# Optimization experiments

Hardware: AMD Instinct MI355X
Metric: run time of the kernel (lower is better)

The kernel has to match this reference:

```python
import jax, jax.numpy as jnp
import numpy as np
from jax import lax


def setup_inputs() -> dict:
    key = jax.random.key(0)
    k1, k2 = jax.random.split(key)
    L, B, D = 1024, 16, 1024
    x = jax.random.normal(k1, (L, B, D), dtype=jnp.float32)
    # weight maps n_in -> n_out*k with k=3 (n_in == n_out); small scale for stability
    weight = jax.random.normal(k2, (D, 3 * D), dtype=jnp.float32) * 0.05
    bias = jnp.zeros((2 * D,), dtype=jnp.float32)
    c0 = jnp.zeros((B, D), dtype=jnp.float32)
    return {"x": x, "weight": weight, "bias": bias, "c0": c0}


def reference(x, weight, bias, c0):
    # SRUCell forward, k == 3 (n_in == n_out), unidirectional, tanh activation,
    # no dropout masks (mask_h == NULL -> mask = 1).
    L, B, D = x.shape
    u = (x.reshape(L * B, D) @ weight).reshape(L, B, D, 3)
    b1 = bias[:D]
    b2 = bias[D:]
    u0 = u[..., 0]                                   # [L, B, D]
    g1 = jax.nn.sigmoid(u[..., 1] + b1)              # forget gate
    g2 = jax.nn.sigmoid(u[..., 2] + b2)              # reset/highway gate

    def step(c, inp):
        u0_t, g1_t, g2_t, x_t = inp
        c_new = (c - u0_t) * g1_t + u0_t             # c = c'*g1 + u0*(1-g1)
        h_t = (jnp.tanh(c_new) - x_t) * g2_t + x_t   # h = act(c)*g2 + x*(1-g2)
        return c_new, h_t

    c_last, h = lax.scan(step, c0, (u0, g1, g2, x))
    return h, c_last
```

## Files before the change

### kernel.cpp

```cpp
#include <hip/hip_runtime.h>

#define L_DIM 1024
#define B_DIM 16
#define D_DIM 1024
#define K_DIM 1024
#define N_DIM 3072
#define M_DIM (L_DIM * B_DIM)
#define CHAINS 16384
#define CHUNK 64
#define NCHUNK 16

typedef float f32x4 __attribute__((ext_vector_type(4)));
typedef __bf16 bf16x8 __attribute__((ext_vector_type(8)));
typedef unsigned short u16;
typedef unsigned int u32;

__device__ __forceinline__ u16 f2bf(float f) {
  u32 u = __float_as_uint(f);
  u = u + 0x7FFFu + ((u >> 16) & 1u);
  return (u16)(u >> 16);
}
__device__ __forceinline__ float bf2f(u16 v) {
  return __uint_as_float(((u32)v) << 16);
}
__device__ __forceinline__ float fexp(float v) {
  return __builtin_amdgcn_exp2f(v * 1.4426950408889634f);
}
__device__ __forceinline__ float sigm(float z) {
  return __builtin_amdgcn_rcpf(1.0f + fexp(-z));
}
__device__ __forceinline__ float ftanh(float v) {
  return 1.0f - 2.0f * __builtin_amdgcn_rcpf(1.0f + fexp(2.0f * v));
}

__global__ __launch_bounds__(256) void cvt_x_kernel(const float4* __restrict__ in,
                                                    ushort4* __restrict__ out, int n4) {
  int i = blockIdx.x * 256 + threadIdx.x;
  if (i < n4) {
    float4 v = in[i];
    ushort4 o;
    o.x = f2bf(v.x); o.y = f2bf(v.y); o.z = f2bf(v.z); o.w = f2bf(v.w);
    out[i] = o;
  }
}

__global__ __launch_bounds__(256) void cvt_w_kernel(const float* __restrict__ W,
                                                    u16* __restrict__ Wt) {
  __shared__ float tile[64][65];
  int c0 = blockIdx.x * 64;
  int r0 = blockIdx.y * 64;
  int tx = threadIdx.x & 63;
  int ty = threadIdx.x >> 6;
#pragma unroll
  for (int i = 0; i < 16; ++i) {
    int row = i * 4 + ty;
    tile[row][tx] = W[(size_t)(r0 + row) * N_DIM + c0 + tx];
  }
  __syncthreads();
#pragma unroll
  for (int i = 0; i < 16; ++i) {
    int crow = i * 4 + ty;
    int c = c0 + crow;
    int nprime = (c % 3) * D_DIM + (c / 3);
    Wt[(size_t)nprime * K_DIM + r0 + tx] = f2bf(tile[tx][crow]);
  }
}

__global__ __launch_bounds__(256) void gemm_kernel(const u16* __restrict__ A,
                                                   const u16* __restrict__ Bt,
                                                   u16* __restrict__ U) {
  __shared__ u16 lA[128 * 32];
  __shared__ u16 lB[128 * 32];
  const int tid = threadIdx.x;
  const int wave = tid >> 6;
  const int lane = tid & 63;
  const int wm = wave >> 1, wn = wave & 1;
  const int quad = lane >> 4, l16 = lane & 15;
  const int m0 = blockIdx.y * 128;
  const int n0 = blockIdx.x * 128;

  f32x4 acc[4][4] = {};

  const u16* gA = A + (size_t)(m0 + (tid >> 2)) * K_DIM + (tid & 3) * 8;
  const u16* gB = Bt + (size_t)(n0 + (tid >> 2)) * K_DIM + (tid & 3) * 8;
  u16* sA0 = lA + wave * 512;
  u16* sA1 = lA + 2048 + wave * 512;
  u16* sB0 = lB + wave * 512;
  u16* sB1 = lB + 2048 + wave * 512;

  const u16* rA = lA + (wm * 64 + l16) * 32 + quad * 8;
  const u16* rB = lB + (wn * 64 + l16) * 32 + quad * 8;

  for (int k0 = 0; k0 < K_DIM; k0 += 32) {
    __syncthreads();
    __builtin_amdgcn_global_load_lds((const __attribute__((address_space(1))) void*)(gA + k0),
                                     (__attribute__((address_space(3))) void*)sA0, 16, 0, 0);
    __builtin_amdgcn_global_load_lds((const __attribute__((address_space(1))) void*)(gA + (size_t)64 * K_DIM + k0),
                                     (__attribute__((address_space(3))) void*)sA1, 16, 0, 0);
    __builtin_amdgcn_global_load_lds((const __attribute__((address_space(1))) void*)(gB + k0),
                                     (__attribute__((address_space(3))) void*)sB0, 16, 0, 0);
    __builtin_amdgcn_global_load_lds((const __attribute__((address_space(1))) void*)(gB + (size_t)64 * K_DIM + k0),
                                     (__attribute__((address_space(3))) void*)sB1, 16, 0, 0);
    __syncthreads();

    bf16x8 af[4], bfr[4];
#pragma unroll
    for (int mt = 0; mt < 4; ++mt) af[mt] = *(const bf16x8*)(rA + mt * 16 * 32);
#pragma unroll
    for (int nt = 0; nt < 4; ++nt) bfr[nt] = *(const bf16x8*)(rB + nt * 16 * 32);
#pragma unroll
    for (int mt = 0; mt < 4; ++mt)
#pragma unroll
      for (int nt = 0; nt < 4; ++nt)
        acc[mt][nt] = __builtin_amdgcn_mfma_f32_16x16x32_bf16(af[mt], bfr[nt], acc[mt][nt], 0, 0, 0);
  }

#pragma unroll
  for (int mt = 0; mt < 4; ++mt) {
#pragma unroll
    for (int nt = 0; nt < 4; ++nt) {
      int col = n0 + wn * 64 + nt * 16 + l16;
      int rbase = m0 + wm * 64 + mt * 16 + quad * 4;
#pragma unroll
      for (int r = 0; r < 4; ++r) {
        U[(size_t)(rbase + r) * N_DIM + col] = f2bf(acc[mt][nt][r]);
      }
    }
  }
}


__global__ __launch_bounds__(256) void sru_phase1(const u16* __restrict__ U,
                                                  const float* __restrict__ bias,
                                                  float* __restrict__ Aarr,
                                                  float* __restrict__ Barr) {
  int tid = blockIdx.x * 256 + threadIdx.x;
  int chain = tid & (CHAINS - 1);
  int j = tid >> 14;
  int d = chain & (D_DIM - 1);
  int b = chain >> 10;
  float bb1 = bias[d];
  const u16* p = U + (size_t)(j * CHUNK * B_DIM + b) * N_DIM + d;
  float A = 1.0f, Bv = 0.0f;
#pragma unroll 4
  for (int s = 0; s < CHUNK; ++s) {
    float u0 = bf2f(p[0]);
    float g1 = sigm(bf2f(p[D_DIM]) + bb1);
    Bv = (Bv - u0) * g1 + u0;
    A *= g1;
    p += (size_t)B_DIM * N_DIM;
  }
  Aarr[tid] = A;
  Barr[tid] = Bv;
}

__global__ __launch_bounds__(256) void sru_phase2(const float* __restrict__ Aarr,
                                                  const float* __restrict__ Barr,
                                                  const float* __restrict__ c0,
                                                  float* __restrict__ Cin,
                                                  float* __restrict__ clast) {
  int chain = blockIdx.x * 256 + threadIdx.x;
  float As[NCHUNK], Bs[NCHUNK];
#pragma unroll
  for (int j = 0; j < NCHUNK; ++j) {
    As[j] = Aarr[j * CHAINS + chain];
    Bs[j] = Barr[j * CHAINS + chain];
  }
  float c = c0[chain];
#pragma unroll
  for (int j = 0; j < NCHUNK; ++j) {
    Cin[j * CHAINS + chain] = c;
    c = As[j] * c + Bs[j];
  }
  clast[chain] = c;
}

__global__ __launch_bounds__(256) void sru_phase3(const u16* __restrict__ U,
                                                  const float* __restrict__ x,
                                                  const float* __restrict__ bias,
                                                  const float* __restrict__ Cin,
                                                  float* __restrict__ h) {
  int tid = blockIdx.x * 256 + threadIdx.x;
  int chain = tid & (CHAINS - 1);
  int j = tid >> 14;
  int d = chain & (D_DIM - 1);
  int b = chain >> 10;
  float bb1 = bias[d];
  float bb2 = bias[D_DIM + d];
  float c = Cin[tid];
  size_t m0 = (size_t)(j * CHUNK * B_DIM + b);
  const u16* p = U + m0 * N_DIM + d;
  const float* xp = x + m0 * D_DIM + d;
  float* hp = h + m0 * D_DIM + d;
#pragma unroll 4
  for (int s = 0; s < CHUNK; ++s) {
    float u0 = bf2f(p[0]);
    float g1 = sigm(bf2f(p[D_DIM]) + bb1);
    float g2 = sigm(bf2f(p[2 * D_DIM]) + bb2);
    c = (c - u0) * g1 + u0;
    float xv = *xp;
    *hp = (ftanh(c) - xv) * g2 + xv;
    p += (size_t)B_DIM * N_DIM;
    xp += B_DIM * D_DIM;
    hp += B_DIM * D_DIM;
  }
}

extern "C" void kernel_launch(void* const* d_in, const int* in_sizes, int n_in,
                              void* d_out, int out_size, void* d_ws, size_t ws_size,
                              hipStream_t stream) {
  const float* x = (const float*)d_in[0];
  const float* W = (const float*)d_in[1];
  const float* bias = (const float*)d_in[2];
  const float* c0 = (const float*)d_in[3];
  float* out = (float*)d_out;

  char* ws = (char*)d_ws;
  u16* xb = (u16*)ws;
  u16* wt = (u16*)(ws + 33554432);
  u16* U = (u16*)(ws + 33554432 + 6291456);
  float* Aarr = (float*)ws;
  float* Barr = (float*)(ws + 1048576);
  float* Cin  = (float*)(ws + 2097152);

  cvt_x_kernel<<<16384, 256, 0, stream>>>((const float4*)x, (ushort4*)xb, M_DIM * K_DIM / 4);
  cvt_w_kernel<<<dim3(48, 16), 256, 0, stream>>>(W, wt);
  gemm_kernel<<<dim3(N_DIM / 128, M_DIM / 128), 256, 0, stream>>>(xb, wt, U);
  sru_phase1<<<CHAINS * NCHUNK / 256, 256, 0, stream>>>(U, bias, Aarr, Barr);
  sru_phase2<<<CHAINS / 256, 256, 0, stream>>>(Aarr, Barr, c0, Cin, out + (size_t)M_DIM * D_DIM);
  sru_phase3<<<CHAINS * NCHUNK / 256, 256, 0, stream>>>(U, x, bias, Cin, out);
}
```

Measured before the change: 298.5 us.

## Rewrite GEMM as 256x256 double-buffered pipelined tile with swizzled LDS

Replaces the simple 128x128, single-buffer, two-barrier-per-K-step GEMM with a 256x256 tile run by 512 threads and a BK of 64. Loads go straight from global memory into a double-buffered LDS layout with an XOR swizzle, and the next tile is prefetched while MFMAs work on the current one. Block ids are remapped so neighbouring blocks share operands in cache, and s_setprio is raised around MFMA bursts. The goal is to hide global-load latency, cut LDS bank conflicts and raise operand reuse per block. The cost is 128KB of LDS and a large accumulator register footprint, and the hand-counted vmcnt waits are fragile.

After: 276.0 us. -7.5%, faster.

```diff
diff --git a/kernel.cpp b/kernel.cpp
--- a/kernel.cpp
+++ b/kernel.cpp
@@ -66,69 +66,140 @@
   }
 }
 
-__global__ __launch_bounds__(256) void gemm_kernel(const u16* __restrict__ A,
-                                                   const u16* __restrict__ Bt,
-                                                   u16* __restrict__ U) {
-  __shared__ u16 lA[128 * 32];
-  __shared__ u16 lB[128 * 32];
+
+#define AS1 __attribute__((address_space(1)))
+#define AS3 __attribute__((address_space(3)))
+#define STAGE(gp, lp) do { \
+  __builtin_amdgcn_global_load_lds((const AS1 void*)(gp), (AS3 void*)(lp), 16, 0, 0); \
+  __builtin_amdgcn_global_load_lds((const AS1 void*)((gp) + (size_t)64 * K_DIM), \
+                                   (AS3 void*)((lp) + 4096), 16, 0, 0); \
+} while (0)
+
+#define QUAD(AI, JB, BF) \
+  _Pragma("unroll") \
+  for (int i = 0; i < 4; ++i) { \
+    _Pragma("unroll") \
+    for (int j = 0; j < 2; ++j) { \
+      acc[AI + i][JB + j] = __builtin_amdgcn_mfma_f32_16x16x32_bf16(aF[i][0], BF[j][0], acc[AI + i][JB + j], 0, 0, 0); \
+      acc[AI + i][JB + j] = __builtin_amdgcn_mfma_f32_16x16x32_bf16(aF[i][1], BF[j][1], acc[AI + i][JB + j], 0, 0, 0); \
+    } \
+  }
+
+__global__ __launch_bounds__(512, 2) void gemm_kernel(const u16* __restrict__ A,
+                                                      const u16* __restrict__ Bt,
+                                                      u16* __restrict__ U) {
+  __shared__ __align__(16) u16 sm[65536];
   const int tid = threadIdx.x;
   const int wave = tid >> 6;
   const int lane = tid & 63;
-  const int wm = wave >> 1, wn = wave & 1;
-  const int quad = lane >> 4, l16 = lane & 15;
-  const int m0 = blockIdx.y * 128;
-  const int n0 = blockIdx.x * 128;
-
-  f32x4 acc[4][4] = {};
-
-  const u16* gA = A + (size_t)(m0 + (tid >> 2)) * K_DIM + (tid & 3) * 8;
-  const u16* gB = Bt + (size_t)(n0 + (tid >> 2)) * K_DIM + (tid & 3) * 8;
-  u16* sA0 = lA + wave * 512;
-  u16* sA1 = lA + 2048 + wave * 512;
-  u16* sB0 = lB + wave * 512;
-  u16* sB1 = lB + 2048 + wave * 512;
-
-  const u16* rA = lA + (wm * 64 + l16) * 32 + quad * 8;
-  const u16* rB = lB + (wn * 64 + l16) * 32 + quad * 8;
-
-  for (int k0 = 0; k0 < K_DIM; k0 += 32) {
-    __syncthreads();
-    __builtin_amdgcn_global_load_lds((const __attribute__((address_space(1))) void*)(gA + k0),
-                                     (__attribute__((address_space(3))) void*)sA0, 16, 0, 0);
-    __builtin_amdgcn_global_load_lds((const __attribute__((address_space(1))) void*)(gA + (size_t)64 * K_DIM + k0),
-                                     (__attribute__((address_space(3))) void*)sA1, 16, 0, 0);
-    __builtin_amdgcn_global_load_lds((const __attribute__((address_space(1))) void*)(gB + k0),
-                                     (__attribute__((address_space(3))) void*)sB0, 16, 0, 0);
-    __builtin_amdgcn_global_load_lds((const __attribute__((address_space(1))) void*)(gB + (size_t)64 * K_DIM + k0),
-                                     (__attribute__((address_space(3))) void*)sB1, 16, 0, 0);
-    __syncthreads();
-
-    bf16x8 af[4], bfr[4];
-#pragma unroll
-    for (int mt = 0; mt < 4; ++mt) af[mt] = *(const bf16x8*)(rA + mt * 16 * 32);
-#pragma unroll
-    for (int nt = 0; nt < 4; ++nt) bfr[nt] = *(const bf16x8*)(rB + nt * 16 * 32);
-#pragma unroll
-    for (int mt = 0; mt < 4; ++mt)
-#pragma unroll
-      for (int nt = 0; nt < 4; ++nt)
-        acc[mt][nt] = __builtin_amdgcn_mfma_f32_16x16x32_bf16(af[mt], bfr[nt], acc[mt][nt], 0, 0, 0);
-  }
-
-#pragma unroll
-  for (int mt = 0; mt < 4; ++mt) {
-#pragma unroll
-    for (int nt = 0; nt < 4; ++nt) {
-      int col = n0 + wn * 64 + nt * 16 + l16;
-      int rbase = m0 + wm * 64 + mt * 16 + quad * 4;
-#pragma unroll
-      for (int r = 0; r < 4; ++r) {
-        U[(size_t)(rbase + r) * N_DIM + col] = f2bf(acc[mt][nt][r]);
-      }
-    }
-  }
-}
-
+  const int wm = wave >> 2;
+  const int wn = wave & 3;
+  const int quad = lane >> 4;
+  const int l16 = lane & 15;
+
+  const int flat = blockIdx.y * 12 + blockIdx.x;
+  const int swz = (flat & 7) * 96 + (flat >> 3);
+  const int m0 = (swz / 12) * 256;
+  const int n0 = (swz % 12) * 256;
+
+  const int rr = tid >> 3;
+  const int slot = (tid & 7) ^ (rr & 7);
+  const u16* gA = A + (size_t)(m0 + rr) * K_DIM + slot * 8;
+  const u16* gB = Bt + (size_t)(n0 + rr) * K_DIM + slot * 8;
+
+  u16* ldsA = sm + wave * 512;
+  u16* ldsB = sm + 32768 + wave * 512;
+
+  const int swzu = (l16 & 7) << 3;
+  const int c0 = (quad * 8) ^ swzu;
+  const int c1 = (32 + quad * 8) ^ swzu;
+  const u16* pA = sm + (wm * 128 + l16) * 64;
+  const u16* pB = sm + 32768 + (wn * 64 + l16) * 64;
+
+  f32x4 acc[8][4] = {};
+
+  STAGE(gA, ldsA);
+  STAGE(gA + (size_t)128 * K_DIM, ldsA + 8192);
+  STAGE(gB, ldsB);
+  STAGE(gB + (size_t)128 * K_DIM, ldsB + 8192);
+  STAGE(gB + 64, ldsB + 16384);
+  STAGE(gB + (size_t)128 * K_DIM + 64, ldsB + 16384 + 8192);
+  asm volatile("s_waitcnt vmcnt(0)" ::: "memory");
+  __builtin_amdgcn_s_barrier();
+
+  for (int u = 0; u < 16; ++u) {
+    const int buf = u & 1;
+    const int nb = buf ^ 1;
+    const u16* pAb = pA + buf * 16384;
+    const u16* pBb = pB + buf * 16384;
+    bf16x8 aF[4][2], bLo[2][2], bHi[2][2];
+
+#pragma unroll
+    for (int i = 0; i < 4; ++i) {
+      aF[i][0] = *(const bf16x8*)(pAb + i * 1024 + c0);
+      aF[i][1] = *(const bf16x8*)(pAb + i * 1024 + c1);
+    }
+#pragma unroll
+    for (int j = 0; j < 2; ++j) {
+      bLo[j][0] = *(const bf16x8*)(pBb + j * 1024 + c0);
+      bLo[j][1] = *(const bf16x8*)(pBb + j * 1024 + c1);
+    }
+    if (u < 15) STAGE(gA + (u + 1) * 64, ldsA + nb * 16384);
+    __builtin_amdgcn_s_barrier();
+    __builtin_amdgcn_s_setprio(1);
+    QUAD(0, 0, bLo)
+    __builtin_amdgcn_s_setprio(0);
+    __builtin_amdgcn_s_barrier();
+
+#pragma unroll
+    for (int j = 0; j < 2; ++j) {
+      bHi[j][0] = *(const bf16x8*)(pBb + (2 + j) * 1024 + c0);
+      bHi[j][1] = *(const bf16x8*)(pBb + (2 + j) * 1024 + c1);
+    }
+    if (u < 15) STAGE(gA + (size_t)128 * K_DIM + (u + 1) * 64, ldsA + nb * 16384 + 8192);
+    __builtin_amdgcn_s_barrier();
+    __builtin_amdgcn_s_setprio(1);
+    QUAD(0, 2, bHi)
+    __builtin_amdgcn_s_setprio(0);
+    __builtin_amdgcn_s_barrier();
+
+#pragma unroll
+    for (int i = 0; i < 4; ++i) {
+      aF[i][0] = *(const bf16x8*)(pAb + (4 + i) * 1024 + c0);
+      aF[i][1] = *(const bf16x8*)(pAb + (4 + i) * 1024 + c1);
+    }
+    if (u < 14) STAGE(gB + (u + 2) * 64, ldsB + buf * 16384);
+    __builtin_amdgcn_s_barrier();
+    __builtin_amdgcn_s_setprio(1);
+    QUAD(4, 2, bHi)
+    __builtin_amdgcn_s_setprio(0);
+    __builtin_amdgcn_s_barrier();
+
+    if (u < 14) {
+      STAGE(gB + (size_t)128 * K_DIM + (u + 2) * 64, ldsB + buf * 16384 + 8192);
+      asm volatile("s_waitcnt vmcnt(4)" ::: "memory");
+    } else if (u == 14) {
+      asm volatile("s_waitcnt vmcnt(0)" ::: "memory");
+    }
+    __builtin_amdgcn_s_barrier();
+    __builtin_amdgcn_s_setprio(1);
+    QUAD(4, 0, bLo)
+    __builtin_amdgcn_s_setprio(0);
+    __builtin_amdgcn_s_barrier();
+  }
+
+#pragma unroll
+  for (int i = 0; i < 8; ++i) {
+#pragma unroll
+    for (int j = 0; j < 4; ++j) {
+      const int col = n0 + wn * 64 + j * 16 + l16;
+      const int rb = m0 + wm * 128 + i * 16 + quad * 4;
+#pragma unroll
+      for (int r = 0; r < 4; ++r)
+        U[(size_t)(rb + r) * N_DIM + col] = f2bf(acc[i][j][r]);
+    }
+  }
+}
 
 __global__ __launch_bounds__(256) void sru_phase1(const u16* __restrict__ U,
                                                   const float* __restrict__ bias,
@@ -225,7 +296,7 @@
 
   cvt_x_kernel<<<16384, 256, 0, stream>>>((const float4*)x, (ushort4*)xb, M_DIM * K_DIM / 4);
   cvt_w_kernel<<<dim3(48, 16), 256, 0, stream>>>(W, wt);
-  gemm_kernel<<<dim3(N_DIM / 128, M_DIM / 128), 256, 0, stream>>>(xb, wt, U);
+  gemm_kernel<<<dim3(N_DIM / 256, M_DIM / 256), 512, 0, stream>>>(xb, wt, U);
   sru_phase1<<<CHAINS * NCHUNK / 256, 256, 0, stream>>>(U, bias, Aarr, Barr);
   sru_phase2<<<CHAINS / 256, 256, 0, stream>>>(Aarr, Barr, c0, Cin, out + (size_t)M_DIM * D_DIM);
   sru_phase3<<<CHAINS * NCHUNK / 256, 256, 0, stream>>>(U, x, bias, Cin, out);
```
